# Kernel optimization log

Measured on AMD Instinct MI355X. Metric: run time of the kernel, lower is better.

## Reference

```python
import jax, jax.numpy as jnp
import numpy as np
from jax import lax


def _conv(x, w, b):
    y = lax.conv_general_dilated(x, w, window_strides=(1, 1), padding='SAME',
                                 dimension_numbers=('NCHW', 'OIHW', 'NCHW'))
    return y + b[None, :, None, None]


def _maxpool2(x):
    return lax.reduce_window(x, -jnp.inf, lax.max,
                             window_dimensions=(1, 1, 2, 2),
                             window_strides=(1, 1, 2, 2), padding='VALID')


def setup_inputs() -> dict:
    key = jax.random.key(0)
    ks = jax.random.split(key, 11)
    f32 = jnp.float32
    return {
        'x': jax.random.normal(ks[0], (512, 1, 112, 112), f32),
        'w_conv1': jax.random.normal(ks[1], (8, 1, 3, 3), f32) * 0.1,
        'b_conv1': jax.random.normal(ks[2], (8,), f32) * 0.1,
        'w_conv2': jax.random.normal(ks[3], (16, 8, 3, 3), f32) * 0.1,
        'b_conv2': jax.random.normal(ks[4], (16,), f32) * 0.1,
        'w_patch': jax.random.normal(ks[5], (4, 64), f32) * 0.1,
        'b_patch': jax.random.normal(ks[6], (4,), f32) * 0.1,
        'w_fc1': jax.random.normal(ks[7], (64, 784), f32) * 0.05,
        'b_fc1': jax.random.normal(ks[8], (64,), f32) * 0.05,
        'w_fc2': jax.random.normal(ks[9], (10, 64), f32) * 0.05,
        'b_fc2': jax.random.normal(ks[10], (10,), f32) * 0.05,
    }


def reference(x, w_conv1, b_conv1, w_conv2, b_conv2, w_patch, b_patch,
              w_fc1, b_fc1, w_fc2, b_fc2):
    B = x.shape[0]
    h = _maxpool2(jax.nn.relu(_conv(x, w_conv1, b_conv1)))        # [B,8,56,56]
    f = _maxpool2(jax.nn.relu(_conv(h, w_conv2, b_conv2)))        # [B,16,28,28]
    C, H, W = f.shape[1], f.shape[2], f.shape[3]
    # im2col: 2x2 non-overlapping spatial patches, flattened as (C,2,2) -> 64
    p = f.reshape(B, C, H // 2, 2, W // 2, 2)
    p = p.transpose(0, 2, 4, 1, 3, 5).reshape(B, (H // 2) * (W // 2), C * 4)  # [B,196,64]
    pf = jnp.einsum('bpk,ok->bpo', p, w_patch) + b_patch          # [B,196,4]
    pf = pf.reshape(B, -1)                                        # [B,784]
    h1 = jax.nn.relu(pf @ w_fc1.T + b_fc1)
    logits = h1 @ w_fc2.T + b_fc2
    return jax.nn.log_softmax(logits, axis=-1)
```

## Files before the change

kernel.cpp:

```cpp
#include <hip/hip_runtime.h>


#define FSTR 33

typedef _Float16 half2_t __attribute__((ext_vector_type(2)));
typedef _Float16 f16x8 __attribute__((ext_vector_type(8)));
typedef float f32x4 __attribute__((ext_vector_type(4)));
typedef float f32x2 __attribute__((ext_vector_type(2)));

__device__ __forceinline__ unsigned pack_f16(float a, float b) {
  union { half2_t h; unsigned u; } z;
  z.h[0] = (_Float16)a;
  z.h[1] = (_Float16)b;
  return z.u;
}

__device__ __forceinline__ half2_t as_h2(unsigned u) {
  union { unsigned u; half2_t h; } z;
  z.u = u;
  return z.h;
}

__device__ __forceinline__ f16x8 as_f16x8(uint4 u) {
  union { uint4 u; f16x8 f; } z;
  z.u = u;
  return z.f;
}

__device__ __forceinline__ float fdot2_(half2_t a, half2_t b, float c) {
#if __has_builtin(__builtin_amdgcn_fdot2)
  return __builtin_amdgcn_fdot2(a, b, c, false);
#else
  return c + (float)a[0] * (float)b[0] + (float)a[1] * (float)b[1];
#endif
}

__global__ __launch_bounds__(256, 6) void k_fused(
    const float* __restrict__ x, const float* __restrict__ w1,
    const float* __restrict__ b1, const float* __restrict__ w2,
    const float* __restrict__ b2, const float* __restrict__ wp,
    const float* __restrict__ bp, const float* __restrict__ w_fc1,
    float* __restrict__ h1p) {
  __shared__ __align__(16) unsigned hsu[3600];
  __shared__ __align__(16) unsigned bwl[768];
  __shared__ __align__(16) unsigned wps[128];
  __shared__ __align__(16) unsigned fsu[49 * FSTR];
  __shared__ __align__(16) float pfl[196];
  const int tid = threadIdx.x;
  const int b = blockIdx.x >> 2;
  const int tile = blockIdx.x & 3;
  const int sr = tile >> 1;
  const int sc = tile & 1;
  const int l = tid & 63;
  const int wv = __builtin_amdgcn_readfirstlane(tid >> 6);
  const float* xb = x + (long)b * 12544;
  const float bpv = bp[tid & 3];

  for (int i = tid; i < 3600; i += 256) hsu[i] = 0u;
  for (int t = tid; t < 768; t += 256) {
    int oc = t / 48, rem = t - oc * 48;
    int tap = rem >> 2, w = rem & 3;
    unsigned v = 0u;
    if (tap < 9)
      v = pack_f16(w2[(oc * 8 + 2 * w) * 9 + tap],
                   w2[(oc * 8 + 2 * w + 1) * 9 + tap]);
    bwl[t] = v;
  }
  if (tid < 128) {
    int i = tid >> 2, ot = tid & 3;
    int l0 = 2 * i, l1 = 2 * i + 1;
    wps[tid] = pack_f16(wp[ot * 64 + (l0 & 15) * 4 + (l0 >> 4)],
                        wp[ot * 64 + (l1 & 15) * 4 + (l1 >> 4)]);
  }
  __syncthreads();

  for (int task = tid; task < 900; task += 256) {
    int r = task / 30, c = task - r * 30;
    int gr = 28 * sr - 1 + r;
    int gc = 28 * sc - 1 + c;
    if ((unsigned)gr >= 56u || (unsigned)gc >= 56u) continue;
    float win[4][4];
    int iy0 = 2 * gr - 1, ix0 = 2 * gc - 1;
    if (gr >= 1 && gr <= 54 && gc >= 1 && gc <= 54) {
      const float* xp = xb + iy0 * 112 + ix0;
#pragma unroll
      for (int rr = 0; rr < 4; ++rr)
#pragma unroll
        for (int qq = 0; qq < 4; ++qq)
          win[rr][qq] = xp[rr * 112 + qq];
    } else {
#pragma unroll
      for (int rr = 0; rr < 4; ++rr) {
        int iy = iy0 + rr;
        bool yok = (unsigned)iy < 112u;
#pragma unroll
        for (int qq = 0; qq < 4; ++qq) {
          int ix = ix0 + qq;
          win[rr][qq] = (yok && (unsigned)ix < 112u) ? xb[iy * 112 + ix] : 0.f;
        }
      }
    }
    float hv[8];
#pragma unroll
    for (int ch = 0; ch < 8; ++ch) {
      f32x2 sA = {0.f, 0.f};
      f32x2 sB = {0.f, 0.f};
#pragma unroll
      for (int ty = 0; ty < 3; ++ty)
#pragma unroll
        for (int tx = 0; tx < 3; ++tx) {
          float wk = w1[ch * 9 + ty * 3 + tx];
          f32x2 wkk = {wk, wk};
          f32x2 xa = {win[ty][tx], win[ty][tx + 1]};
          f32x2 xb2 = {win[ty + 1][tx], win[ty + 1][tx + 1]};
          sA = __builtin_elementwise_fma(xa, wkk, sA);
          sB = __builtin_elementwise_fma(xb2, wkk, sB);
        }
      f32x2 sm = __builtin_elementwise_max(sA, sB);
      float m = fmaxf(sm.x, sm.y);
      hv[ch] = fmaxf(m + b1[ch], 0.f);
    }
    uint4 hw;
    hw.x = pack_f16(hv[0], hv[1]);
    hw.y = pack_f16(hv[2], hv[3]);
    hw.z = pack_f16(hv[4], hv[5]);
    hw.w = pack_f16(hv[6], hv[7]);
    *(uint4*)(hsu + (r * 30 + c) * 4) = hw;
  }
  __syncthreads();

  {
    const int q = l >> 4;
    const int yoff = 2 * ((l >> 3) & 1) + ((l >> 1) & 1);
    const int xoff = 2 * ((l >> 2) & 1) + (l & 1);
    int poff[3];
#pragma unroll
    for (int kk = 0; kk < 3; ++kk) {
      int t = kk * 4 + q;
      int tt = t < 9 ? t : 8;
      int ty = tt / 3, tx = tt - ty * 3;
      poff[kk] = ((yoff + ty) * 30 + xoff + tx) * 4;
    }
    uint4 bu0 = *(const uint4*)(bwl + ((l & 15) * 12 + 0 + q) * 4);
    uint4 bu1 = *(const uint4*)(bwl + ((l & 15) * 12 + 4 + q) * 4);
    uint4 bu2 = *(const uint4*)(bwl + ((l & 15) * 12 + 8 + q) * 4);
    const float b2v = b2[l & 15];
    _Float16* fsh = (_Float16*)fsu;

#pragma unroll 2
    for (int p_l = wv; p_l < 49; p_l += 4) {
      int py = p_l / 7, px = p_l - py * 7;
      int pb = 480 * py + 16 * px;
      uint4 a0u = *(const uint4*)(hsu + pb + poff[0]);
      uint4 a1u = *(const uint4*)(hsu + pb + poff[1]);
      uint4 a2u = *(const uint4*)(hsu + pb + poff[2]);
      f32x4 acc = {0.f, 0.f, 0.f, 0.f};
      acc = __builtin_amdgcn_mfma_f32_16x16x32_f16(as_f16x8(a0u), as_f16x8(bu0), acc, 0, 0, 0);
      acc = __builtin_amdgcn_mfma_f32_16x16x32_f16(as_f16x8(a1u), as_f16x8(bu1), acc, 0, 0, 0);
      acc = __builtin_amdgcn_mfma_f32_16x16x32_f16(as_f16x8(a2u), as_f16x8(bu2), acc, 0, 0, 0);
      float mx = fmaxf(fmaxf(acc[0], acc[1]), fmaxf(acc[2], acc[3]));
      float fv = fmaxf(mx + b2v, 0.f);
      fsh[p_l * (2 * FSTR) + l] = (_Float16)fv;
    }
    __syncthreads();
    if (tid < 196) {
      int row = tid >> 2, ot = tid & 3;
      const unsigned* fr = fsu + row * FSTR;
      float acc = 0.f;
#pragma unroll
      for (int i = 0; i < 32; ++i)
        acc = fdot2_(as_h2(fr[i]), as_h2(wps[i * 4 + ot]), acc);
      pfl[row * 4 + ot] = acc + bpv;
    }
    __syncthreads();
  }

  {
    int j = tid >> 2, q4 = tid & 3;
    const float* wrow = w_fc1 + j * 784;
    float acc = 0.f;
#pragma unroll 4
    for (int lp = q4; lp < 49; lp += 4) {
      int Pl = lp / 7, Ql = lp - Pl * 7;
      int gp = (7 * sr + Pl) * 14 + 7 * sc + Ql;
      float4 w4 = *(const float4*)(wrow + gp * 4);
      float4 p4 = *(const float4*)(pfl + lp * 4);
      acc += w4.x * p4.x + w4.y * p4.y + w4.z * p4.z + w4.w * p4.w;
    }
    acc += __shfl_down(acc, 2, 4);
    acc += __shfl_down(acc, 1, 4);
    if (q4 == 0) h1p[((long)b * 4 + tile) * 64 + j] = acc;
  }
}

__global__ __launch_bounds__(256) void k_tail(const float* __restrict__ h1p,
                                              const float* __restrict__ b_fc1,
                                              const float* __restrict__ w_fc2,
                                              const float* __restrict__ b_fc2,
                                              float* __restrict__ out) {
  const int l = threadIdx.x & 63;
  const int wv = threadIdx.x >> 6;
  const int b = blockIdx.x * 4 + wv;
  const float* hp = h1p + (long)b * 256;
  float v = b_fc1[l] + hp[l] + hp[64 + l] + hp[128 + l] + hp[192 + l];
  float h = fmaxf(v, 0.f);
  float lg[10];
#pragma unroll
  for (int o = 0; o < 10; ++o) {
    float t = h * w_fc2[o * 64 + l];
#pragma unroll
    for (int off = 32; off; off >>= 1) t += __shfl_xor(t, off);
    lg[o] = t + b_fc2[o];
  }
  float mx = lg[0];
#pragma unroll
  for (int o = 1; o < 10; ++o) mx = fmaxf(mx, lg[o]);
  float se = 0.f;
#pragma unroll
  for (int o = 0; o < 10; ++o) se += __expf(lg[o] - mx);
  float ls = mx + __logf(se);
#pragma unroll
  for (int o = 0; o < 10; ++o)
    if (l == o) out[b * 10 + o] = lg[o] - ls;
}

extern "C" void kernel_launch(void* const* d_in, const int* in_sizes, int n_in,
                              void* d_out, int out_size, void* d_ws, size_t ws_size,
                              hipStream_t stream) {
  const float* x = (const float*)d_in[0];
  const float* w1 = (const float*)d_in[1];
  const float* b1 = (const float*)d_in[2];
  const float* w2 = (const float*)d_in[3];
  const float* b2 = (const float*)d_in[4];
  const float* wp = (const float*)d_in[5];
  const float* bp = (const float*)d_in[6];
  const float* wf1 = (const float*)d_in[7];
  const float* bf1 = (const float*)d_in[8];
  const float* wf2 = (const float*)d_in[9];
  const float* bf2 = (const float*)d_in[10];

  float* h1p = (float*)d_ws;

  k_fused<<<dim3(2048), 256, 0, stream>>>(x, w1, b1, w2, b2, wp, bp, wf1, h1p);
  k_tail<<<dim3(128), 256, 0, stream>>>(h1p, bf1, wf2, bf2, (float*)d_out);
}
```

Measured before the change: 117.8 us.

## Fuse whole network into one kernel with one 1024-thread block per image

Replaces the four-tile-per-image conv kernel and the separate tail kernel with one kernel where a 1024-thread block processes a whole image, including fc1, fc2 and log_softmax. This removes the halo recomputation between tiles, the second launch and the partial-sum round trip through global memory. Only the padding border of the shared buffer is zeroed instead of the whole buffer. In exchange the grid drops to 512 large blocks with about 58 KB of shared memory each, which reduces occupancy and scheduling flexibility across CUs, and the final logits step runs on one wave while the other waves sit idle.

```diff
diff --git a/kernel.cpp b/kernel.cpp
--- a/kernel.cpp
+++ b/kernel.cpp
@@ -1,6 +1,7 @@
 #include <hip/hip_runtime.h>
 
 
+#define HS 58
 #define FSTR 33
 
 typedef _Float16 half2_t __attribute__((ext_vector_type(2)));
@@ -35,30 +36,36 @@
 #endif
 }
 
-__global__ __launch_bounds__(256, 6) void k_fused(
+__global__ __launch_bounds__(1024, 8) void k_all(
     const float* __restrict__ x, const float* __restrict__ w1,
     const float* __restrict__ b1, const float* __restrict__ w2,
     const float* __restrict__ b2, const float* __restrict__ wp,
     const float* __restrict__ bp, const float* __restrict__ w_fc1,
-    float* __restrict__ h1p) {
-  __shared__ __align__(16) unsigned hsu[3600];
+    const float* __restrict__ b_fc1, const float* __restrict__ w_fc2,
+    const float* __restrict__ b_fc2, float* __restrict__ out) {
+  __shared__ __align__(16) unsigned hsu[HS * HS * 4];
   __shared__ __align__(16) unsigned bwl[768];
   __shared__ __align__(16) unsigned wps[128];
-  __shared__ __align__(16) unsigned fsu[49 * FSTR];
-  __shared__ __align__(16) float pfl[196];
+  __shared__ __align__(16) unsigned fsu[98 * FSTR];
+  __shared__ __align__(16) float pfl[784];
+  __shared__ float h1s[64];
   const int tid = threadIdx.x;
-  const int b = blockIdx.x >> 2;
-  const int tile = blockIdx.x & 3;
-  const int sr = tile >> 1;
-  const int sc = tile & 1;
+  const int b = blockIdx.x;
   const int l = tid & 63;
   const int wv = __builtin_amdgcn_readfirstlane(tid >> 6);
   const float* xb = x + (long)b * 12544;
   const float bpv = bp[tid & 3];
 
-  for (int i = tid; i < 3600; i += 256) hsu[i] = 0u;
-  for (int t = tid; t < 768; t += 256) {
-    int oc = t / 48, rem = t - oc * 48;
+  if (tid < 228) {
+    int i = tid, hr, hc;
+    if (i < 58) { hr = 0; hc = i; }
+    else if (i < 116) { hr = 57; hc = i - 58; }
+    else if (i < 172) { hr = i - 115; hc = 0; }
+    else { hr = i - 171; hc = 57; }
+    *(uint4*)(hsu + (hr * HS + hc) * 4) = make_uint4(0u, 0u, 0u, 0u);
+  }
+  if (tid < 768) {
+    int t = tid, oc = t / 48, rem = t - oc * 48;
     int tap = rem >> 2, w = rem & 3;
     unsigned v = 0u;
     if (tap < 9)
@@ -66,19 +73,16 @@
                    w2[(oc * 8 + 2 * w + 1) * 9 + tap]);
     bwl[t] = v;
   }
-  if (tid < 128) {
-    int i = tid >> 2, ot = tid & 3;
+  if (tid >= 768 && tid < 896) {
+    int t = tid - 768;
+    int i = t >> 2, ot = t & 3;
     int l0 = 2 * i, l1 = 2 * i + 1;
-    wps[tid] = pack_f16(wp[ot * 64 + (l0 & 15) * 4 + (l0 >> 4)],
-                        wp[ot * 64 + (l1 & 15) * 4 + (l1 >> 4)]);
-  }
-  __syncthreads();
-
-  for (int task = tid; task < 900; task += 256) {
-    int r = task / 30, c = task - r * 30;
-    int gr = 28 * sr - 1 + r;
-    int gc = 28 * sc - 1 + c;
-    if ((unsigned)gr >= 56u || (unsigned)gc >= 56u) continue;
+    wps[t] = pack_f16(wp[ot * 64 + (l0 & 15) * 4 + (l0 >> 4)],
+                      wp[ot * 64 + (l1 & 15) * 4 + (l1 >> 4)]);
+  }
+
+  for (int task = tid; task < 3136; task += 1024) {
+    int gr = task / 56, gc = task - gr * 56;
     float win[4][4];
     int iy0 = 2 * gr - 1, ix0 = 2 * gc - 1;
     if (gr >= 1 && gr <= 54 && gc >= 1 && gc <= 54) {
@@ -125,7 +129,7 @@
     hw.y = pack_f16(hv[2], hv[3]);
     hw.z = pack_f16(hv[4], hv[5]);
     hw.w = pack_f16(hv[6], hv[7]);
-    *(uint4*)(hsu + (r * 30 + c) * 4) = hw;
+    *(uint4*)(hsu + ((gr + 1) * HS + gc + 1) * 4) = hw;
   }
   __syncthreads();
 
@@ -139,7 +143,7 @@
       int t = kk * 4 + q;
       int tt = t < 9 ? t : 8;
       int ty = tt / 3, tx = tt - ty * 3;
-      poff[kk] = ((yoff + ty) * 30 + xoff + tx) * 4;
+      poff[kk] = ((yoff + ty) * HS + xoff + tx) * 4;
     }
     uint4 bu0 = *(const uint4*)(bwl + ((l & 15) * 12 + 0 + q) * 4);
     uint4 bu1 = *(const uint4*)(bwl + ((l & 15) * 12 + 4 + q) * 4);
@@ -147,81 +151,75 @@
     const float b2v = b2[l & 15];
     _Float16* fsh = (_Float16*)fsu;
 
+    for (int c = 0; c < 2; ++c) {
 #pragma unroll 2
-    for (int p_l = wv; p_l < 49; p_l += 4) {
-      int py = p_l / 7, px = p_l - py * 7;
-      int pb = 480 * py + 16 * px;
-      uint4 a0u = *(const uint4*)(hsu + pb + poff[0]);
-      uint4 a1u = *(const uint4*)(hsu + pb + poff[1]);
-      uint4 a2u = *(const uint4*)(hsu + pb + poff[2]);
-      f32x4 acc = {0.f, 0.f, 0.f, 0.f};
-      acc = __builtin_amdgcn_mfma_f32_16x16x32_f16(as_f16x8(a0u), as_f16x8(bu0), acc, 0, 0, 0);
-      acc = __builtin_amdgcn_mfma_f32_16x16x32_f16(as_f16x8(a1u), as_f16x8(bu1), acc, 0, 0, 0);
-      acc = __builtin_amdgcn_mfma_f32_16x16x32_f16(as_f16x8(a2u), as_f16x8(bu2), acc, 0, 0, 0);
-      float mx = fmaxf(fmaxf(acc[0], acc[1]), fmaxf(acc[2], acc[3]));
-      float fv = fmaxf(mx + b2v, 0.f);
-      fsh[p_l * (2 * FSTR) + l] = (_Float16)fv;
-    }
-    __syncthreads();
-    if (tid < 196) {
-      int row = tid >> 2, ot = tid & 3;
-      const unsigned* fr = fsu + row * FSTR;
-      float acc = 0.f;
-#pragma unroll
-      for (int i = 0; i < 32; ++i)
-        acc = fdot2_(as_h2(fr[i]), as_h2(wps[i * 4 + ot]), acc);
-      pfl[row * 4 + ot] = acc + bpv;
-    }
-    __syncthreads();
+      for (int p_l = wv; p_l < 98; p_l += 16) {
+        int p = c * 98 + p_l;
+        int py = p / 14, px = p - py * 14;
+        int pb = (4 * py * HS + 4 * px) * 4;
+        uint4 a0u = *(const uint4*)(hsu + pb + poff[0]);
+        uint4 a1u = *(const uint4*)(hsu + pb + poff[1]);
+        uint4 a2u = *(const uint4*)(hsu + pb + poff[2]);
+        f32x4 acc = {0.f, 0.f, 0.f, 0.f};
+        acc = __builtin_amdgcn_mfma_f32_16x16x32_f16(as_f16x8(a0u), as_f16x8(bu0), acc, 0, 0, 0);
+        acc = __builtin_amdgcn_mfma_f32_16x16x32_f16(as_f16x8(a1u), as_f16x8(bu1), acc, 0, 0, 0);
+        acc = __builtin_amdgcn_mfma_f32_16x16x32_f16(as_f16x8(a2u), as_f16x8(bu2), acc, 0, 0, 0);
+        float mx = fmaxf(fmaxf(acc[0], acc[1]), fmaxf(acc[2], acc[3]));
+        float fv = fmaxf(mx + b2v, 0.f);
+        fsh[p_l * (2 * FSTR) + l] = (_Float16)fv;
+      }
+      __syncthreads();
+      if (tid < 392) {
+        int row = tid >> 2, ot = tid & 3;
+        const unsigned* fr = fsu + row * FSTR;
+        float acc = 0.f;
+#pragma unroll
+        for (int i = 0; i < 32; ++i)
+          acc = fdot2_(as_h2(fr[i]), as_h2(wps[i * 4 + ot]), acc);
+        pfl[(c * 98 + row) * 4 + ot] = acc + bpv;
+      }
+      __syncthreads();
+    }
   }
 
   {
-    int j = tid >> 2, q4 = tid & 3;
+    int j = tid >> 4, q16 = tid & 15;
     const float* wrow = w_fc1 + j * 784;
     float acc = 0.f;
-#pragma unroll 4
-    for (int lp = q4; lp < 49; lp += 4) {
-      int Pl = lp / 7, Ql = lp - Pl * 7;
-      int gp = (7 * sr + Pl) * 14 + 7 * sc + Ql;
-      float4 w4 = *(const float4*)(wrow + gp * 4);
+    for (int lp = q16; lp < 196; lp += 16) {
+      float4 w4 = *(const float4*)(wrow + lp * 4);
       float4 p4 = *(const float4*)(pfl + lp * 4);
       acc += w4.x * p4.x + w4.y * p4.y + w4.z * p4.z + w4.w * p4.w;
     }
-    acc += __shfl_down(acc, 2, 4);
-    acc += __shfl_down(acc, 1, 4);
-    if (q4 == 0) h1p[((long)b * 4 + tile) * 64 + j] = acc;
-  }
-}
-
-__global__ __launch_bounds__(256) void k_tail(const float* __restrict__ h1p,
-                                              const float* __restrict__ b_fc1,
-                                              const float* __restrict__ w_fc2,
-                                              const float* __restrict__ b_fc2,
-                                              float* __restrict__ out) {
-  const int l = threadIdx.x & 63;
-  const int wv = threadIdx.x >> 6;
-  const int b = blockIdx.x * 4 + wv;
-  const float* hp = h1p + (long)b * 256;
-  float v = b_fc1[l] + hp[l] + hp[64 + l] + hp[128 + l] + hp[192 + l];
-  float h = fmaxf(v, 0.f);
-  float lg[10];
-#pragma unroll
-  for (int o = 0; o < 10; ++o) {
-    float t = h * w_fc2[o * 64 + l];
-#pragma unroll
-    for (int off = 32; off; off >>= 1) t += __shfl_xor(t, off);
-    lg[o] = t + b_fc2[o];
-  }
-  float mx = lg[0];
-#pragma unroll
-  for (int o = 1; o < 10; ++o) mx = fmaxf(mx, lg[o]);
-  float se = 0.f;
-#pragma unroll
-  for (int o = 0; o < 10; ++o) se += __expf(lg[o] - mx);
-  float ls = mx + __logf(se);
-#pragma unroll
-  for (int o = 0; o < 10; ++o)
-    if (l == o) out[b * 10 + o] = lg[o] - ls;
+    acc += __shfl_down(acc, 8, 16);
+    acc += __shfl_down(acc, 4, 16);
+    acc += __shfl_down(acc, 2, 16);
+    acc += __shfl_down(acc, 1, 16);
+    if (q16 == 0) h1s[j] = fmaxf(acc + b_fc1[j], 0.f);
+  }
+  __syncthreads();
+
+  if (wv == 0) {
+    float h = h1s[l];
+    float lg[10];
+#pragma unroll
+    for (int o = 0; o < 10; ++o) {
+      float t = h * w_fc2[o * 64 + l];
+#pragma unroll
+      for (int off = 32; off; off >>= 1) t += __shfl_xor(t, off);
+      lg[o] = t + b_fc2[o];
+    }
+    float mx = lg[0];
+#pragma unroll
+    for (int o = 1; o < 10; ++o) mx = fmaxf(mx, lg[o]);
+    float se = 0.f;
+#pragma unroll
+    for (int o = 0; o < 10; ++o) se += __expf(lg[o] - mx);
+    float ls = mx + __logf(se);
+#pragma unroll
+    for (int o = 0; o < 10; ++o)
+      if (l == o) out[b * 10 + o] = lg[o] - ls;
+  }
 }
 
 extern "C" void kernel_launch(void* const* d_in, const int* in_sizes, int n_in,
@@ -238,9 +236,8 @@
   const float* bf1 = (const float*)d_in[8];
   const float* wf2 = (const float*)d_in[9];
   const float* bf2 = (const float*)d_in[10];
-
-  float* h1p = (float*)d_ws;
-
-  k_fused<<<dim3(2048), 256, 0, stream>>>(x, w1, b1, w2, b2, wp, bp, wf1, h1p);
-  k_tail<<<dim3(128), 256, 0, stream>>>(h1p, bf1, wf2, bf2, (float*)d_out);
-}
+  (void)d_ws; (void)ws_size;
+
+  k_all<<<dim3(512), 1024, 0, stream>>>(x, w1, b1, w2, b2, wp, bp, wf1, bf1,
+                                        wf2, bf2, (float*)d_out);
+}
```

New measurement: 116.4 us. About the same (-1.2%).
